# Kernel tuning notes

Measured on AMD Instinct MI355X. Metric: run time of the kernel, lower is better.

The kernel has to match this reference:

```python
import jax, jax.numpy as jnp
import numpy as np


def _hfft3(x):
    # sequential Hermitian FFT along the 3 spatial axes; each axis n -> 2*(n-1)
    for ax in (2, 3, 4):
        x = jnp.fft.hfft(x, axis=ax)
    return x


def _ihfft3(x):
    # sequential inverse Hermitian FFT; ihfft requires real input, so take real
    # part before each application (mirrors numpy semantics on the original code)
    for ax in (2, 3, 4):
        x = jnp.fft.ihfft(jnp.real(x), axis=ax)
    return x


def setup_inputs() -> dict:
    key = jax.random.key(0)
    k1, k2 = jax.random.split(key)
    B, Cin, Cout = 4, 32, 32
    D1 = D2 = D3 = 64
    m1 = m2 = m3 = 16
    scale = 1.0 / (Cin * Cout)
    x = jax.random.normal(k1, (B, Cin, D1, D2, D3), dtype=jnp.float32)
    weights1 = scale * jax.random.uniform(k2, (Cin, Cout, m1, m2, m3), dtype=jnp.float32)
    return {"x": x, "weights1": weights1}


def reference(x, weights1):
    B = x.shape[0]
    D1, D2, D3 = x.shape[2], x.shape[3], x.shape[4]
    Cout = weights1.shape[1]
    m1, m2, m3 = weights1.shape[2], weights1.shape[3], weights1.shape[4]

    # 3D Hartley-style transform: [B,Cin,2(D1-1),2(D2-1),2(D3-1)] real
    x_ht = _hfft3(x)

    # mode truncation + channel mixing on low modes only
    low = jnp.einsum("bixyz,ioxyz->boxyz", x_ht[:, :, :m1, :m2, :m3], weights1)

    out_ht = jnp.zeros((B, Cout, D1, D2, D3 // 2 + 1), dtype=x.dtype)
    out_ht = out_ht.at[:, :, :m1, :m2, :m3].set(low)

    # inverse transform -> complex [B,Cout,D1//2+1,D2//2+1,(D3//2+1)//2+1]
    out = _ihfft3(out_ht)
    # return real/imag stacked so output is real-valued
    return jnp.stack([out.real, out.imag], axis=-1)
```

## Files before the change

kernel.cpp:

```cpp
#include <hip/hip_runtime.h>


#define PI2 6.283185307179586476925f

__global__ __launch_bounds__(256) void k_fwd12(const float* __restrict__ x,
                                               float* __restrict__ A2,
                                               float* __restrict__ cA,
                                               float* __restrict__ cB,
                                               float* __restrict__ sB) {
    __shared__ float xt[64 * 68];
    __shared__ float Ts[16 * 68];
    __shared__ float tmp[16 * 68];
    const int j1 = blockIdx.x, bc = blockIdx.y;
    const int t = threadIdx.x;

    float4* xt4 = (float4*)xt;
    float4* Ts4 = (float4*)Ts;
    const float4* xg = (const float4*)(x + ((size_t)bc * 64 + j1) * 4096);
    for (int c = t; c < 1024; c += 256) {
        int j2 = c >> 4, q = c & 15;
        xt4[j2 * 17 + q] = xg[c];
    }
    {
        int k = t >> 4, q = t & 15;
        float4 tv;
        float* tp = (float*)&tv;
#pragma unroll
        for (int e = 0; e < 4; e++) {
            int j = 4 * q + e;
            float w = (j == 0 || j == 63) ? 1.f : 2.f;
            int r = (j * k) % 126;
            tp[e] = w * cosf(PI2 * (float)r / 126.f);
        }
        Ts4[k * 17 + q] = tv;
    }
    if (j1 == 0 && bc == 0) {
        for (int c = t; c < 528; c += 256) {
            int p = c >> 4, j = c & 15;
            int r = (j * p) % 64;
            cA[c] = cosf(PI2 * (float)r / 64.f) * (1.f / 64.f);
        }
        for (int c = t; c < 272; c += 256) {
            int p = c >> 4, j = c & 15;
            int r = (j * p) % 33;
            float a = PI2 * (float)r / 33.f;
            cB[c] = cosf(a) * (1.f / 33.f);
            sB[c] = sinf(a) * (1.f / 33.f);
        }
    }
    __syncthreads();

    {
        const int j2l = t & 31;
        const int k3l = t >> 5;
        float a00 = 0.f, a01 = 0.f, a10 = 0.f, a11 = 0.f;
#pragma unroll 4
        for (int q = 0; q < 16; q++) {
            float4 x0 = xt4[j2l * 17 + q];
            float4 x1 = xt4[(j2l + 32) * 17 + q];
            float4 t0 = Ts4[k3l * 17 + q];
            float4 t1 = Ts4[(k3l + 8) * 17 + q];
            a00 += x0.x * t0.x + x0.y * t0.y + x0.z * t0.z + x0.w * t0.w;
            a01 += x0.x * t1.x + x0.y * t1.y + x0.z * t1.z + x0.w * t1.w;
            a10 += x1.x * t0.x + x1.y * t0.y + x1.z * t0.z + x1.w * t0.w;
            a11 += x1.x * t1.x + x1.y * t1.y + x1.z * t1.z + x1.w * t1.w;
        }
        tmp[k3l * 68 + j2l] = a00;
        tmp[(k3l + 8) * 68 + j2l] = a01;
        tmp[k3l * 68 + j2l + 32] = a10;
        tmp[(k3l + 8) * 68 + j2l + 32] = a11;
    }
    __syncthreads();

    {
        const int k3 = t & 15;
        const int k2 = t >> 4;
        const float4* tmp4 = (const float4*)tmp;
        float acc = 0.f;
#pragma unroll 4
        for (int q = 0; q < 16; q++) {
            float4 tv = tmp4[k3 * 17 + q];
            float4 Tv = Ts4[k2 * 17 + q];
            acc += tv.x * Tv.x + tv.y * Tv.y + tv.z * Tv.z + tv.w * Tv.w;
        }
        A2[((size_t)bc * 64 + j1) * 256 + t] = acc;
    }
}

__global__ __launch_bounds__(256) void k_fwd3(const float* __restrict__ A2,
                                              float* __restrict__ X) {
    __shared__ float Tst[512];
    const int k1h = blockIdx.x;
    const int bc = blockIdx.y;
    const int t = threadIdx.x;
    for (int c0 = t; c0 < 512; c0 += 256) {
        int j1 = c0 >> 3, c = c0 & 7;
        int k1 = k1h * 8 + c;
        float w = (j1 == 0 || j1 == 63) ? 1.f : 2.f;
        int r = (j1 * k1) % 126;
        Tst[c0] = w * cosf(PI2 * (float)r / 126.f);
    }
    __syncthreads();
    const float* Ap = A2 + (size_t)bc * 64 * 256 + t;
    float acc[8] = {0.f, 0.f, 0.f, 0.f, 0.f, 0.f, 0.f, 0.f};
#pragma unroll 8
    for (int j1 = 0; j1 < 64; j1++) {
        float v = Ap[j1 * 256];
        float4 t0 = *(const float4*)&Tst[j1 * 8];
        float4 t1 = *(const float4*)&Tst[j1 * 8 + 4];
        acc[0] += v * t0.x; acc[1] += v * t0.y; acc[2] += v * t0.z; acc[3] += v * t0.w;
        acc[4] += v * t1.x; acc[5] += v * t1.y; acc[6] += v * t1.z; acc[7] += v * t1.w;
    }
    float* Xp = X + (size_t)bc * 4096 + (size_t)(k1h * 8) * 256 + t;
#pragma unroll
    for (int c = 0; c < 8; c++) Xp[(size_t)c * 256] = acc[c];
}

__global__ __launch_bounds__(256) void k_mix(const float* __restrict__ X,
                                             const float* __restrict__ W,
                                             float* __restrict__ low) {
    const int mc = blockIdx.x;
    const int og = blockIdx.y;
    const int m = mc * 256 + threadIdx.x;
    const float* Xp = X + m;
    const float* Wp = W + (size_t)(og * 2) * 4096 + m;
    float acc[4][2] = {{0.f,0.f},{0.f,0.f},{0.f,0.f},{0.f,0.f}};
#pragma unroll 4
    for (int i = 0; i < 32; i++) {
        float w0 = Wp[(size_t)(i * 32) * 4096];
        float w1 = Wp[(size_t)(i * 32 + 1) * 4096];
#pragma unroll
        for (int b = 0; b < 4; b++) {
            float xv = Xp[(size_t)(b * 32 + i) * 4096];
            acc[b][0] += xv * w0;
            acc[b][1] += xv * w1;
        }
    }
#pragma unroll
    for (int b = 0; b < 4; b++) {
        low[((size_t)(b * 32 + og * 2)) * 4096 + m] = acc[b][0];
        low[((size_t)(b * 32 + og * 2 + 1)) * 4096 + m] = acc[b][1];
    }
}

__global__ __launch_bounds__(256) void k_inv(const float* __restrict__ low,
                                             const float* __restrict__ cA,
                                             const float* __restrict__ cB,
                                             const float* __restrict__ sB,
                                             float* __restrict__ out) {
    __shared__ float lt[4096];
    __shared__ float c1[3 * 256];
    __shared__ float c2[3 * 528];
    __shared__ float cAs[528], cBs[272], sBs[272];
    const int p1b = blockIdx.x * 3;
    const int bo = blockIdx.y;
    const int t = threadIdx.x;

    float4* lt4 = (float4*)lt;
    const float4* lg = (const float4*)(low + (size_t)bo * 4096);
    for (int c = t; c < 1024; c += 256) lt4[c] = lg[c];
    for (int c = t; c < 528; c += 256) cAs[c] = cA[c];
    for (int c = t; c < 272; c += 256) { cBs[c] = cB[c]; sBs[c] = sB[c]; }
    __syncthreads();

    {
        float e0 = 0.f, e1 = 0.f, e2 = 0.f;
#pragma unroll
        for (int k1 = 0; k1 < 16; k1++) {
            float v = lt[(k1 << 8) + t];
            e0 += v * cAs[(p1b + 0) * 16 + k1];
            e1 += v * cAs[(p1b + 1) * 16 + k1];
            e2 += v * cAs[(p1b + 2) * 16 + k1];
        }
        c1[t] = e0; c1[256 + t] = e1; c1[512 + t] = e2;
    }
    __syncthreads();

    for (int idx = t; idx < 528; idx += 256) {
        int p2 = idx >> 4, k3 = idx & 15;
        float f0 = 0.f, f1 = 0.f, f2 = 0.f;
#pragma unroll
        for (int k2 = 0; k2 < 16; k2++) {
            float cv = cAs[p2 * 16 + k2];
            int a = (k2 << 4) + k3;
            f0 += c1[a] * cv;
            f1 += c1[256 + a] * cv;
            f2 += c1[512 + a] * cv;
        }
        c2[idx] = f0; c2[528 + idx] = f1; c2[1056 + idx] = f2;
    }
    __syncthreads();

    for (int s = 0; s < 3; s++) {
        float* op = out + ((size_t)bo * 33 + p1b + s) * 33 * 17 * 2;
        const float* c2p = c2 + s * 528;
        for (int idx = t; idx < 1122; idx += 256) {
            int p2 = idx / 34, rem = idx - p2 * 34;
            int p3 = rem >> 1, cc = rem & 1;
            const float* M = cc ? sBs : cBs;
            float acc = 0.f;
#pragma unroll
            for (int k3 = 0; k3 < 16; k3++) acc += c2p[(p2 << 4) + k3] * M[p3 * 16 + k3];
            op[idx] = acc;
        }
    }
}

extern "C" void kernel_launch(void* const* d_in, const int* in_sizes, int n_in,
                              void* d_out, int out_size, void* d_ws, size_t ws_size,
                              hipStream_t stream) {
    const float* x = (const float*)d_in[0];
    const float* W = (const float*)d_in[1];
    float* out = (float*)d_out;

    float* ws = (float*)d_ws;
    float* cA   = ws;
    float* cB   = ws + 528;
    float* sB   = ws + 800;
    float* A2   = ws + 4096;
    float* X    = A2 + 2097152;
    float* low  = X + 524288;

    k_fwd12<<<dim3(64, 128), dim3(256), 0, stream>>>(x, A2, cA, cB, sB);
    k_fwd3<<<dim3(2, 128), dim3(256), 0, stream>>>(A2, X);
    k_mix<<<dim3(16, 16), dim3(256), 0, stream>>>(X, W, low);
    k_inv<<<dim3(11, 128), dim3(256), 0, stream>>>(low, cA, cB, sB, out);
}
```

Measured before the change: 239.2 us.

## Fuse third forward transform axis into first kernel with split-j1 partial sums

The separate axis-1 transform kernel goes away. Each forward block now loops over 16 j1 slices, register-prefetches the next slice, and accumulates the 16 low k1 modes in registers. The four j1-quarter partial sums go to a partials buffer and are added together inside the mixing kernel's loads. This removes the A2 intermediate round trip and one launch. In exchange there are fewer, longer blocks (512 blocks instead of 8192), more serialized syncs, and four times as many loads in the mix kernel.

```diff
diff --git a/kernel.cpp b/kernel.cpp
--- a/kernel.cpp
+++ b/kernel.cpp
@@ -3,24 +3,26 @@
 
 #define PI2 6.283185307179586476925f
 
-__global__ __launch_bounds__(256) void k_fwd12(const float* __restrict__ x,
-                                               float* __restrict__ A2,
-                                               float* __restrict__ cA,
-                                               float* __restrict__ cB,
-                                               float* __restrict__ sB) {
+__global__ __launch_bounds__(256) void k_fwd(const float* __restrict__ x,
+                                             float* __restrict__ Xp,
+                                             float* __restrict__ cA,
+                                             float* __restrict__ cB,
+                                             float* __restrict__ sB) {
     __shared__ float xt[64 * 68];
     __shared__ float Ts[16 * 68];
     __shared__ float tmp[16 * 68];
-    const int j1 = blockIdx.x, bc = blockIdx.y;
+    const int j1q = blockIdx.x;
+    const int bc = blockIdx.y;
     const int t = threadIdx.x;
 
     float4* xt4 = (float4*)xt;
     float4* Ts4 = (float4*)Ts;
-    const float4* xg = (const float4*)(x + ((size_t)bc * 64 + j1) * 4096);
-    for (int c = t; c < 1024; c += 256) {
-        int j2 = c >> 4, q = c & 15;
-        xt4[j2 * 17 + q] = xg[c];
-    }
+
+    const float4* xg = (const float4*)x + ((size_t)bc * 64 + j1q * 16) * 1024;
+    float4 buf[4], nxt[4];
+#pragma unroll
+    for (int c = 0; c < 4; c++) buf[c] = xg[c * 256 + t];
+
     {
         int k = t >> 4, q = t & 15;
         float4 tv;
@@ -34,7 +36,7 @@
         }
         Ts4[k * 17 + q] = tv;
     }
-    if (j1 == 0 && bc == 0) {
+    if (j1q == 0 && bc == 0) {
         for (int c = t; c < 528; c += 256) {
             int p = c >> 4, j = c & 15;
             int r = (j * p) % 64;
@@ -48,81 +50,76 @@
             sB[c] = sinf(a) * (1.f / 33.f);
         }
     }
-    __syncthreads();
-
-    {
-        const int j2l = t & 31;
-        const int k3l = t >> 5;
-        float a00 = 0.f, a01 = 0.f, a10 = 0.f, a11 = 0.f;
+
+    float acc[16];
+#pragma unroll
+    for (int k1 = 0; k1 < 16; k1++) acc[k1] = 0.f;
+
+    for (int i = 0; i < 16; i++) {
+        if (i < 15) {
+#pragma unroll
+            for (int c = 0; c < 4; c++) nxt[c] = xg[(i + 1) * 1024 + c * 256 + t];
+        }
+#pragma unroll
+        for (int c = 0; c < 4; c++) {
+            int e = c * 256 + t;
+            xt4[(e >> 4) * 17 + (e & 15)] = buf[c];
+        }
+        __syncthreads();
+
+        {
+            const int j2l = t & 31;
+            const int k3l = t >> 5;
+            float a00 = 0.f, a01 = 0.f, a10 = 0.f, a11 = 0.f;
 #pragma unroll 4
-        for (int q = 0; q < 16; q++) {
-            float4 x0 = xt4[j2l * 17 + q];
-            float4 x1 = xt4[(j2l + 32) * 17 + q];
-            float4 t0 = Ts4[k3l * 17 + q];
-            float4 t1 = Ts4[(k3l + 8) * 17 + q];
-            a00 += x0.x * t0.x + x0.y * t0.y + x0.z * t0.z + x0.w * t0.w;
-            a01 += x0.x * t1.x + x0.y * t1.y + x0.z * t1.z + x0.w * t1.w;
-            a10 += x1.x * t0.x + x1.y * t0.y + x1.z * t0.z + x1.w * t0.w;
-            a11 += x1.x * t1.x + x1.y * t1.y + x1.z * t1.z + x1.w * t1.w;
-        }
-        tmp[k3l * 68 + j2l] = a00;
-        tmp[(k3l + 8) * 68 + j2l] = a01;
-        tmp[k3l * 68 + j2l + 32] = a10;
-        tmp[(k3l + 8) * 68 + j2l + 32] = a11;
-    }
-    __syncthreads();
-
-    {
-        const int k3 = t & 15;
-        const int k2 = t >> 4;
-        const float4* tmp4 = (const float4*)tmp;
-        float acc = 0.f;
+            for (int q = 0; q < 16; q++) {
+                float4 x0 = xt4[j2l * 17 + q];
+                float4 x1 = xt4[(j2l + 32) * 17 + q];
+                float4 t0 = Ts4[k3l * 17 + q];
+                float4 t1 = Ts4[(k3l + 8) * 17 + q];
+                a00 += x0.x * t0.x + x0.y * t0.y + x0.z * t0.z + x0.w * t0.w;
+                a01 += x0.x * t1.x + x0.y * t1.y + x0.z * t1.z + x0.w * t1.w;
+                a10 += x1.x * t0.x + x1.y * t0.y + x1.z * t0.z + x1.w * t0.w;
+                a11 += x1.x * t1.x + x1.y * t1.y + x1.z * t1.z + x1.w * t1.w;
+            }
+            tmp[k3l * 68 + j2l] = a00;
+            tmp[(k3l + 8) * 68 + j2l] = a01;
+            tmp[k3l * 68 + j2l + 32] = a10;
+            tmp[(k3l + 8) * 68 + j2l + 32] = a11;
+        }
+        __syncthreads();
+
+        {
+            const int k3 = t & 15;
+            const int k2 = t >> 4;
+            const float4* tmp4 = (const float4*)tmp;
+            float a2 = 0.f;
 #pragma unroll 4
-        for (int q = 0; q < 16; q++) {
-            float4 tv = tmp4[k3 * 17 + q];
-            float4 Tv = Ts4[k2 * 17 + q];
-            acc += tv.x * Tv.x + tv.y * Tv.y + tv.z * Tv.z + tv.w * Tv.w;
-        }
-        A2[((size_t)bc * 64 + j1) * 256 + t] = acc;
-    }
-}
-
-__global__ __launch_bounds__(256) void k_fwd3(const float* __restrict__ A2,
-                                              float* __restrict__ X) {
-    __shared__ float Tst[512];
-    const int k1h = blockIdx.x;
-    const int bc = blockIdx.y;
-    const int t = threadIdx.x;
-    for (int c0 = t; c0 < 512; c0 += 256) {
-        int j1 = c0 >> 3, c = c0 & 7;
-        int k1 = k1h * 8 + c;
-        float w = (j1 == 0 || j1 == 63) ? 1.f : 2.f;
-        int r = (j1 * k1) % 126;
-        Tst[c0] = w * cosf(PI2 * (float)r / 126.f);
-    }
-    __syncthreads();
-    const float* Ap = A2 + (size_t)bc * 64 * 256 + t;
-    float acc[8] = {0.f, 0.f, 0.f, 0.f, 0.f, 0.f, 0.f, 0.f};
-#pragma unroll 8
-    for (int j1 = 0; j1 < 64; j1++) {
-        float v = Ap[j1 * 256];
-        float4 t0 = *(const float4*)&Tst[j1 * 8];
-        float4 t1 = *(const float4*)&Tst[j1 * 8 + 4];
-        acc[0] += v * t0.x; acc[1] += v * t0.y; acc[2] += v * t0.z; acc[3] += v * t0.w;
-        acc[4] += v * t1.x; acc[5] += v * t1.y; acc[6] += v * t1.z; acc[7] += v * t1.w;
-    }
-    float* Xp = X + (size_t)bc * 4096 + (size_t)(k1h * 8) * 256 + t;
-#pragma unroll
-    for (int c = 0; c < 8; c++) Xp[(size_t)c * 256] = acc[c];
-}
-
-__global__ __launch_bounds__(256) void k_mix(const float* __restrict__ X,
+            for (int q = 0; q < 16; q++) {
+                float4 tv = tmp4[k3 * 17 + q];
+                float4 Tv = Ts4[k2 * 17 + q];
+                a2 += tv.x * Tv.x + tv.y * Tv.y + tv.z * Tv.z + tv.w * Tv.w;
+            }
+            const int j1 = j1q * 16 + i;
+#pragma unroll
+            for (int k1 = 0; k1 < 16; k1++) acc[k1] += a2 * Ts[k1 * 68 + j1];
+        }
+#pragma unroll
+        for (int c = 0; c < 4; c++) buf[c] = nxt[c];
+    }
+
+    float* Xo = Xp + (size_t)j1q * 524288 + (size_t)bc * 4096 + t;
+#pragma unroll
+    for (int k1 = 0; k1 < 16; k1++) Xo[(size_t)k1 * 256] = acc[k1];
+}
+
+__global__ __launch_bounds__(256) void k_mix(const float* __restrict__ Xp,
                                              const float* __restrict__ W,
                                              float* __restrict__ low) {
     const int mc = blockIdx.x;
     const int og = blockIdx.y;
     const int m = mc * 256 + threadIdx.x;
-    const float* Xp = X + m;
+    const float* Xb = Xp + m;
     const float* Wp = W + (size_t)(og * 2) * 4096 + m;
     float acc[4][2] = {{0.f,0.f},{0.f,0.f},{0.f,0.f},{0.f,0.f}};
 #pragma unroll 4
@@ -131,7 +128,9 @@
         float w1 = Wp[(size_t)(i * 32 + 1) * 4096];
 #pragma unroll
         for (int b = 0; b < 4; b++) {
-            float xv = Xp[(size_t)(b * 32 + i) * 4096];
+            size_t off = (size_t)(b * 32 + i) * 4096;
+            float xv = (Xb[off] + Xb[524288 + off]) +
+                       (Xb[1048576 + off] + Xb[1572864 + off]);
             acc[b][0] += xv * w0;
             acc[b][1] += xv * w1;
         }
@@ -217,12 +216,10 @@
     float* cA   = ws;
     float* cB   = ws + 528;
     float* sB   = ws + 800;
-    float* A2   = ws + 4096;
-    float* X    = A2 + 2097152;
-    float* low  = X + 524288;
-
-    k_fwd12<<<dim3(64, 128), dim3(256), 0, stream>>>(x, A2, cA, cB, sB);
-    k_fwd3<<<dim3(2, 128), dim3(256), 0, stream>>>(A2, X);
-    k_mix<<<dim3(16, 16), dim3(256), 0, stream>>>(X, W, low);
+    float* Xp   = ws + 4096;
+    float* low  = Xp + 2097152;
+
+    k_fwd<<<dim3(4, 128), dim3(256), 0, stream>>>(x, Xp, cA, cB, sB);
+    k_mix<<<dim3(16, 16), dim3(256), 0, stream>>>(Xp, W, low);
     k_inv<<<dim3(11, 128), dim3(256), 0, stream>>>(low, cA, cB, sB, out);
 }
```

After: 306.2 us. +28.0%, slower.
